# Kernel optimization log

Measured on AMD Instinct MI355X. Metric: run time of the kernel, lower is better.

The kernel has to match this reference:

```python
import jax, jax.numpy as jnp
import numpy as np

N, F, HOPS, HID, NCLS = 100000, 128, 8, 256, 64

def prelu(x, a):
    return jnp.where(x >= 0, x, a * x)

def setup_inputs() -> dict:
    key = jax.random.key(0)
    ks = jax.random.split(key, 8)
    w = lambda i, shape: (jax.random.normal(ks[i], shape, dtype=jnp.float32) * 0.02)
    return {
        "feats": jax.random.normal(ks[0], (HOPS, N, F), dtype=jnp.float32),
        # lr_jk_ref: Dense(HOPS*F, HID) -> PReLU(a_jk) -> Dense(HID, HID)
        "W_jk1": w(1, (HOPS * F, HID)), "b_jk1": jnp.zeros((HID,), jnp.float32),
        "W_jk2": w(2, (HID, HID)),      "b_jk2": jnp.zeros((HID,), jnp.float32),
        # PReLU params (nn.PReLU default init 0.25): FFN-internal, module-level, output-FFN
        "a_jk": jnp.float32(0.25), "a_main": jnp.float32(0.25), "a_out": jnp.float32(0.25),
        # lr_att: Linear(HID + F, 1), split into the jk_ref part and the per-hop x part
        "w_att_ref": w(3, (HID,)), "w_att_x": w(4, (F,)), "b_att": jnp.zeros((), jnp.float32),
        # lr_output: Dense(F, HID) -> PReLU(a_out) -> Dense(HID, NCLS)
        "W_o1": w(5, (F, HID)),  "b_o1": jnp.zeros((HID,), jnp.float32),
        "W_o2": w(6, (HID, NCLS)), "b_o2": jnp.zeros((NCLS,), jnp.float32),
    }

def reference(feats, W_jk1, b_jk1, W_jk2, b_jk2, a_jk, a_main, a_out,
              w_att_ref, w_att_x, b_att, W_o1, b_o1, W_o2, b_o2):
    # feats: [HOPS, N, F]; dropouts are identity (rates = 0 / eval mode)
    n = feats.shape[1]
    # torch.cat(input_list, dim=1) -> [N, HOPS*F]
    concat = jnp.transpose(feats, (1, 0, 2)).reshape(n, -1)
    # lr_jk_ref (FeedForwardNetII, n_layers=2): Dense -> PReLU -> Dense, then module PReLU
    h = prelu(concat @ W_jk1 + b_jk1, a_jk)
    jk_ref = prelu(h @ W_jk2 + b_jk2, a_main)              # [N, HID]
    # attention scores: sigmoid(Linear(cat(jk_ref, x_i))) for each hop i, vectorized
    s_ref = jk_ref @ w_att_ref                              # [N]
    s_x = jnp.einsum('hnf,f->nh', feats, w_att_x)           # [N, HOPS]
    scores = jax.nn.sigmoid(s_x + s_ref[:, None] + b_att)   # [N, HOPS]
    Wsm = jax.nn.softmax(scores, axis=1)                    # softmax over hops
    # weighted multi-hop aggregation: sum_i W[:,i] * x_i
    agg = jnp.einsum('nh,hnf->nf', Wsm, feats)              # [N, F]
    # lr_output (FeedForwardNetII, n_layers=2): Dense -> PReLU -> Dense
    out = prelu(agg @ W_o1 + b_o1, a_out) @ W_o2 + b_o2     # [N, NCLS]
    return out
```

## Files before the change

### kernel.cpp

```cpp
#include <hip/hip_runtime.h>
#include <hip/hip_bf16.h>
#include <cstdint>
#include <cstddef>

#define N_F 128
#define N_HOPS 8
#define N_HID 256
#define N_CLS 64

typedef __bf16 bf16;
typedef __attribute__((ext_vector_type(8))) __bf16 bf16x8;
typedef __attribute__((ext_vector_type(4))) float f32x4;

__device__ inline f32x4 mfma16(bf16x8 a, bf16x8 b, f32x4 c) {
    return __builtin_amdgcn_mfma_f32_16x16x32_bf16(a, b, c, 0, 0, 0);
}

typedef const __attribute__((address_space(1))) unsigned int guint;
typedef __attribute__((address_space(3))) unsigned int luint;
__device__ __forceinline__ void gl_lds16(const void* g, void* l) {
    __builtin_amdgcn_global_load_lds((guint*)g, (luint*)l, 16, 0, 0);
}

__device__ inline void pack_one(const float* __restrict__ s, bf16* __restrict__ d,
                                int NC, int ntn, int idx) {
    const int lane = idx & 63;
    const int f = idx >> 6;
    const int kt = f / ntn, nt = f - kt * ntn;
    const int krow = kt * 32 + ((lane >> 4) << 3);
    const int col = nt * 16 + (lane & 15);
    const float* ss = s + (size_t)krow * NC + col;
    bf16* dd = d + ((size_t)f * 64 + lane) * 8;
#pragma unroll
    for (int j = 0; j < 8; ++j) dd[j] = (bf16)ss[(size_t)j * NC];
}

__global__ void pack_weights(const float* __restrict__ W1, const float* __restrict__ W2,
                             const float* __restrict__ O1, const float* __restrict__ O2,
                             bf16* p1, bf16* p2, bf16* p3, bf16* p4) {
    int i = blockIdx.x * 256 + threadIdx.x;
    if (i < 32768) { pack_one(W1, p1, 256, 16, i); return; }
    i -= 32768;
    if (i < 8192)  { pack_one(W2, p2, 256, 16, i); return; }
    i -= 8192;
    if (i < 4096)  { pack_one(O1, p3, 256, 16, i); return; }
    i -= 4096;
    if (i < 2048)  { pack_one(O2, p4, 64, 4, i); return; }
}

__global__ __launch_bounds__(256) void k1_kernel(
    const float* __restrict__ feats, const bf16* __restrict__ w1p, const bf16* __restrict__ w2p,
    const float* __restrict__ b1, const float* __restrict__ b2,
    const float* __restrict__ a_jk_p, const float* __restrict__ a_main_p,
    const float* __restrict__ wref, const float* __restrict__ wax,
    const float* __restrict__ batt_p,
    float* __restrict__ wsm, int N)
{
    union __align__(16) U1 {
        struct { bf16 A[2048]; bf16 B[8192]; } s;
        bf16 H[64 * 264];
    };
    __shared__ U1 u;
    __shared__ float sx[64 * 8];
    __shared__ float sref[64];

    const int t = threadIdx.x;
    const int lane = t & 63;
    const int wc = t >> 6;
    const int row0 = blockIdx.x * 64;

    for (int i = t; i < 64 * 8; i += 256) sx[i] = 0.f;
    if (t < 64) sref[t] = 0.f;
    __syncthreads();

    const int srow = t & 63;
    const int sc = t >> 6;
    const int grow = min(row0 + srow, N - 1);

    f32x4 acc[4][4] = {};
    float pacc = 0.f;

    for (int kt = 0; kt < 32; ++kt) {
        const int h = kt >> 2;
        const int f0 = ((kt & 3) << 5) + (sc << 3);
        const float* srcp = feats + ((size_t)h * N + grow) * N_F + f0;
        const float4 v0 = *(const float4*)srcp;
        const float4 v1 = *(const float4*)(srcp + 4);
        pacc += v0.x * wax[f0]     + v0.y * wax[f0 + 1] + v0.z * wax[f0 + 2] + v0.w * wax[f0 + 3]
              + v1.x * wax[f0 + 4] + v1.y * wax[f0 + 5] + v1.z * wax[f0 + 6] + v1.w * wax[f0 + 7];
        if ((kt & 3) == 3) { atomicAdd(&sx[srow * 8 + h], pacc); pacc = 0.f; }
        bf16x8 av;
        av[0] = (bf16)v0.x; av[1] = (bf16)v0.y; av[2] = (bf16)v0.z; av[3] = (bf16)v0.w;
        av[4] = (bf16)v1.x; av[5] = (bf16)v1.y; av[6] = (bf16)v1.z; av[7] = (bf16)v1.w;
        *(bf16x8*)&u.s.A[((((srow >> 4) << 6) + (sc << 4) + (srow & 15))) << 3] = av;
        const bf16* bsrc = w1p + (size_t)kt * 8192;
#pragma unroll
        for (int r = 0; r < 4; ++r)
            gl_lds16(bsrc + r * 2048 + t * 8, &u.s.B[r * 2048 + t * 8]);
        __syncthreads();
        bf16x8 af[4], bfr[4];
#pragma unroll
        for (int i = 0; i < 4; ++i) af[i] = *(bf16x8*)&u.s.A[((i << 6) + lane) << 3];
#pragma unroll
        for (int j = 0; j < 4; ++j) bfr[j] = *(bf16x8*)&u.s.B[(((wc << 2) + j) * 64 + lane) << 3];
#pragma unroll
        for (int i = 0; i < 4; ++i)
#pragma unroll
            for (int j = 0; j < 4; ++j)
                acc[i][j] = mfma16(af[i], bfr[j], acc[i][j]);
        __syncthreads();
    }

    const float ajk = *a_jk_p;
#pragma unroll
    for (int j = 0; j < 4; ++j) {
        const int colg = (wc << 6) + (j << 4) + (lane & 15);
        const float bias = b1[colg];
#pragma unroll
        for (int i = 0; i < 4; ++i)
#pragma unroll
            for (int r = 0; r < 4; ++r) {
                const int row = (i << 4) + ((lane >> 4) << 2) + r;
                float v = acc[i][j][r] + bias;
                v = v >= 0.f ? v : ajk * v;
                u.H[row * 264 + colg] = (bf16)v;
            }
    }
    __syncthreads();

    f32x4 acc2[4][4] = {};
    for (int kt = 0; kt < 8; ++kt) {
        bf16x8 af[4], bfr[4];
#pragma unroll
        for (int i = 0; i < 4; ++i)
            af[i] = *(bf16x8*)&u.H[((i << 4) + (lane & 15)) * 264 + (kt << 5) + ((lane >> 4) << 3)];
#pragma unroll
        for (int j = 0; j < 4; ++j)
            bfr[j] = *(const bf16x8*)&w2p[((size_t)((kt << 4) + (wc << 2) + j) * 64 + lane) * 8];
#pragma unroll
        for (int i = 0; i < 4; ++i)
#pragma unroll
            for (int j = 0; j < 4; ++j)
                acc2[i][j] = mfma16(af[i], bfr[j], acc2[i][j]);
    }

    const float amain = *a_main_p;
    float pr[4][4] = {};
#pragma unroll
    for (int j = 0; j < 4; ++j) {
        const int colg = (wc << 6) + (j << 4) + (lane & 15);
        const float bias = b2[colg];
        const float wr_ = wref[colg];
#pragma unroll
        for (int i = 0; i < 4; ++i)
#pragma unroll
            for (int r = 0; r < 4; ++r) {
                float v = acc2[i][j][r] + bias;
                v = v >= 0.f ? v : amain * v;
                pr[i][r] += v * wr_;
            }
    }
#pragma unroll
    for (int m = 1; m < 16; m <<= 1)
#pragma unroll
        for (int i = 0; i < 4; ++i)
#pragma unroll
            for (int r = 0; r < 4; ++r)
                pr[i][r] += __shfl_xor(pr[i][r], m, 64);
    if ((lane & 15) == 0) {
#pragma unroll
        for (int i = 0; i < 4; ++i)
#pragma unroll
            for (int r = 0; r < 4; ++r)
                atomicAdd(&sref[(i << 4) + ((lane >> 4) << 2) + r], pr[i][r]);
    }
    __syncthreads();

    if (t < 64) {
        const int rg = row0 + t;
        if (rg < N) {
            const float sr = sref[t] + *batt_p;
            float e[8], mx = -1e30f;
#pragma unroll
            for (int h = 0; h < 8; ++h) {
                const float s = 1.f / (1.f + expf(-(sx[t * 8 + h] + sr)));
                e[h] = s; mx = fmaxf(mx, s);
            }
            float sum = 0.f;
#pragma unroll
            for (int h = 0; h < 8; ++h) { e[h] = expf(e[h] - mx); sum += e[h]; }
            const float inv = 1.f / sum;
#pragma unroll
            for (int h = 0; h < 8; ++h) wsm[(size_t)rg * 8 + h] = e[h] * inv;
        }
    }
}

__global__ __launch_bounds__(256) void k2_kernel(
    const float* __restrict__ feats, const float* __restrict__ wsm,
    const bf16* __restrict__ o1p, const bf16* __restrict__ o2p,
    const float* __restrict__ bo1, const float* __restrict__ a_out_p,
    const float* __restrict__ bo2, float* __restrict__ out, int N)
{
    union __align__(16) U2 {
        bf16 AG[64 * 136];
        bf16 HO[64 * 264];
    };
    __shared__ U2 u;
    __shared__ float wsl[512];

    const int t = threadIdx.x;
    const int lane = t & 63;
    const int cg = t >> 6;
    const int row0 = blockIdx.x * 64;

    for (int i = t; i < 512; i += 256) {
        const int rg = min(row0 + (i >> 3), N - 1);
        wsl[i] = wsm[(size_t)rg * 8 + (i & 7)];
    }
    __syncthreads();

    {
        const int r = t >> 2;
        const int c = t & 3;
        const int rg = min(row0 + r, N - 1);
        f32x4 a4[8] = {};
#pragma unroll
        for (int h = 0; h < 8; ++h) {
            const float wgt = wsl[r * 8 + h];
            const f32x4* p4 = (const f32x4*)(feats + ((size_t)h * N + rg) * N_F + c * 32);
#pragma unroll
            for (int q = 0; q < 8; ++q) a4[q] += wgt * p4[q];
        }
#pragma unroll
        for (int q2 = 0; q2 < 4; ++q2) {
            bf16x8 av;
#pragma unroll
            for (int e = 0; e < 4; ++e) {
                av[e] = (bf16)a4[q2 * 2][e];
                av[4 + e] = (bf16)a4[q2 * 2 + 1][e];
            }
            *(bf16x8*)&u.AG[r * 136 + c * 32 + q2 * 8] = av;
        }
    }
    __syncthreads();

    f32x4 acc3[4][4] = {};
    for (int kt = 0; kt < 4; ++kt) {
        bf16x8 af[4], bfr[4];
#pragma unroll
        for (int i = 0; i < 4; ++i)
            af[i] = *(bf16x8*)&u.AG[((i << 4) + (lane & 15)) * 136 + (kt << 5) + ((lane >> 4) << 3)];
#pragma unroll
        for (int j = 0; j < 4; ++j)
            bfr[j] = *(const bf16x8*)&o1p[((size_t)((kt << 4) + (cg << 2) + j) * 64 + lane) * 8];
#pragma unroll
        for (int i = 0; i < 4; ++i)
#pragma unroll
            for (int j = 0; j < 4; ++j)
                acc3[i][j] = mfma16(af[i], bfr[j], acc3[i][j]);
    }
    __syncthreads();

    const float aout = *a_out_p;
#pragma unroll
    for (int j = 0; j < 4; ++j) {
        const int colg = (cg << 6) + (j << 4) + (lane & 15);
        const float bias = bo1[colg];
#pragma unroll
        for (int i = 0; i < 4; ++i)
#pragma unroll
            for (int r = 0; r < 4; ++r) {
                const int row = (i << 4) + ((lane >> 4) << 2) + r;
                float v = acc3[i][j][r] + bias;
                v = v >= 0.f ? v : aout * v;
                u.HO[row * 264 + colg] = (bf16)v;
            }
    }
    __syncthreads();

    f32x4 acc4[4] = {};
    for (int kt = 0; kt < 8; ++kt) {
        const bf16x8 b = *(const bf16x8*)&o2p[((size_t)((kt << 2) + cg) * 64 + lane) * 8];
#pragma unroll
        for (int i = 0; i < 4; ++i) {
            const bf16x8 a = *(bf16x8*)&u.HO[((i << 4) + (lane & 15)) * 264 + (kt << 5) + ((lane >> 4) << 3)];
            acc4[i] = mfma16(a, b, acc4[i]);
        }
    }
    {
        const int colg = (cg << 4) + (lane & 15);
        const float bv = bo2[colg];
#pragma unroll
        for (int i = 0; i < 4; ++i)
#pragma unroll
            for (int r = 0; r < 4; ++r) {
                const int rg = row0 + (i << 4) + ((lane >> 4) << 2) + r;
                if (rg < N) out[(size_t)rg * 64 + colg] = acc4[i][r] + bv;
            }
    }
}

extern "C" void kernel_launch(void* const* d_in, const int* in_sizes, int n_in,
                              void* d_out, int out_size, void* d_ws, size_t ws_size,
                              hipStream_t stream) {
    const float* feats  = (const float*)d_in[0];
    const float* W1     = (const float*)d_in[1];
    const float* b1     = (const float*)d_in[2];
    const float* W2     = (const float*)d_in[3];
    const float* b2     = (const float*)d_in[4];
    const float* a_jk   = (const float*)d_in[5];
    const float* a_main = (const float*)d_in[6];
    const float* a_out  = (const float*)d_in[7];
    const float* wref   = (const float*)d_in[8];
    const float* wax    = (const float*)d_in[9];
    const float* batt   = (const float*)d_in[10];
    const float* O1     = (const float*)d_in[11];
    const float* bo1    = (const float*)d_in[12];
    const float* O2     = (const float*)d_in[13];
    const float* bo2    = (const float*)d_in[14];

    const int N = in_sizes[0] / (N_HOPS * N_F);

    char* ws = (char*)d_ws;
    bf16* p1 = (bf16*)ws;
    bf16* p2 = (bf16*)(ws + 524288);
    bf16* p3 = (bf16*)(ws + 655360);
    bf16* p4 = (bf16*)(ws + 720896);
    float* wsm = (float*)(ws + 753664);

    pack_weights<<<184, 256, 0, stream>>>(W1, W2, O1, O2, p1, p2, p3, p4);
    const int nb = (N + 63) / 64;
    k1_kernel<<<nb, 256, 0, stream>>>(feats, p1, p2, b1, b2, a_jk, a_main,
                                      wref, wax, batt, wsm, N);
    k2_kernel<<<nb, 256, 0, stream>>>(feats, wsm, p3, p4, bo1, a_out, bo2,
                                      (float*)d_out, N);
}
```

Baseline: 762.5 us.

## Load feats directly into MFMA fragments per wave and drop LDS staging in k1

In k1, each wave now loads its own A fragments of feats straight from global memory and its B fragments of W1 straight from global memory. This removes the shared A/B staging buffers and the two barriers per k-step. The attention dot product with w_att_x is split across waves by hop and reduced with shuffles instead of LDS atomics. The hidden activations in both kernels are stored in a fragment-ordered LDS layout so that MFMA operand reads become contiguous. The trade-off is that all four waves now read the same feats rows, giving 4x redundant global/L2 reads of the dominant input, in exchange for no block-level synchronization.

```diff
diff --git a/kernel.cpp b/kernel.cpp
--- a/kernel.cpp
+++ b/kernel.cpp
@@ -14,12 +14,6 @@
 
 __device__ inline f32x4 mfma16(bf16x8 a, bf16x8 b, f32x4 c) {
     return __builtin_amdgcn_mfma_f32_16x16x32_bf16(a, b, c, 0, 0, 0);
-}
-
-typedef const __attribute__((address_space(1))) unsigned int guint;
-typedef __attribute__((address_space(3))) unsigned int luint;
-__device__ __forceinline__ void gl_lds16(const void* g, void* l) {
-    __builtin_amdgcn_global_load_lds((guint*)g, (luint*)l, 16, 0, 0);
 }
 
 __device__ inline void pack_one(const float* __restrict__ s, bf16* __restrict__ d,
@@ -48,6 +42,10 @@
     if (i < 2048)  { pack_one(O2, p4, 64, 4, i); return; }
 }
 
+__device__ __forceinline__ int frag_addr(int row, int col) {
+    return (((col >> 5) << 2) + (row >> 4)) * 512 + (((row & 15) | (((col >> 3) & 3) << 4)) << 3) + (col & 7);
+}
+
 __global__ __launch_bounds__(256) void k1_kernel(
     const float* __restrict__ feats, const bf16* __restrict__ w1p, const bf16* __restrict__ w2p,
     const float* __restrict__ b1, const float* __restrict__ b2,
@@ -56,11 +54,7 @@
     const float* __restrict__ batt_p,
     float* __restrict__ wsm, int N)
 {
-    union __align__(16) U1 {
-        struct { bf16 A[2048]; bf16 B[8192]; } s;
-        bf16 H[64 * 264];
-    };
-    __shared__ U1 u;
+    __shared__ bf16 Hf[32 * 512];
     __shared__ float sx[64 * 8];
     __shared__ float sref[64];
 
@@ -68,62 +62,77 @@
     const int lane = t & 63;
     const int wc = t >> 6;
     const int row0 = blockIdx.x * 64;
-
-    for (int i = t; i < 64 * 8; i += 256) sx[i] = 0.f;
+    const int m = lane & 15, q = lane >> 4;
+
     if (t < 64) sref[t] = 0.f;
-    __syncthreads();
-
-    const int srow = t & 63;
-    const int sc = t >> 6;
-    const int grow = min(row0 + srow, N - 1);
+
+    size_t rbase[4];
+#pragma unroll
+    for (int i = 0; i < 4; ++i) {
+        const int r = min(row0 + (i << 4) + m, N - 1);
+        rbase[i] = (size_t)r * N_F;
+    }
 
     f32x4 acc[4][4] = {};
-    float pacc = 0.f;
+    float pacc[4] = {};
 
     for (int kt = 0; kt < 32; ++kt) {
         const int h = kt >> 2;
-        const int f0 = ((kt & 3) << 5) + (sc << 3);
-        const float* srcp = feats + ((size_t)h * N + grow) * N_F + f0;
-        const float4 v0 = *(const float4*)srcp;
-        const float4 v1 = *(const float4*)(srcp + 4);
-        pacc += v0.x * wax[f0]     + v0.y * wax[f0 + 1] + v0.z * wax[f0 + 2] + v0.w * wax[f0 + 3]
-              + v1.x * wax[f0 + 4] + v1.y * wax[f0 + 5] + v1.z * wax[f0 + 6] + v1.w * wax[f0 + 7];
-        if ((kt & 3) == 3) { atomicAdd(&sx[srow * 8 + h], pacc); pacc = 0.f; }
-        bf16x8 av;
-        av[0] = (bf16)v0.x; av[1] = (bf16)v0.y; av[2] = (bf16)v0.z; av[3] = (bf16)v0.w;
-        av[4] = (bf16)v1.x; av[5] = (bf16)v1.y; av[6] = (bf16)v1.z; av[7] = (bf16)v1.w;
-        *(bf16x8*)&u.s.A[((((srow >> 4) << 6) + (sc << 4) + (srow & 15))) << 3] = av;
-        const bf16* bsrc = w1p + (size_t)kt * 8192;
-#pragma unroll
-        for (int r = 0; r < 4; ++r)
-            gl_lds16(bsrc + r * 2048 + t * 8, &u.s.B[r * 2048 + t * 8]);
-        __syncthreads();
-        bf16x8 af[4], bfr[4];
-#pragma unroll
-        for (int i = 0; i < 4; ++i) af[i] = *(bf16x8*)&u.s.A[((i << 6) + lane) << 3];
-#pragma unroll
-        for (int j = 0; j < 4; ++j) bfr[j] = *(bf16x8*)&u.s.B[(((wc << 2) + j) * 64 + lane) << 3];
+        const int f0 = ((kt & 3) << 5) + (q << 3);
+        const size_t hoff = (size_t)h * N * N_F;
+        bf16x8 af[4];
+        float4 v0s[4], v1s[4];
+#pragma unroll
+        for (int i = 0; i < 4; ++i) {
+            const float* p = feats + hoff + rbase[i] + f0;
+            const float4 v0 = *(const float4*)p;
+            const float4 v1 = *(const float4*)(p + 4);
+            v0s[i] = v0; v1s[i] = v1;
+            af[i][0] = (bf16)v0.x; af[i][1] = (bf16)v0.y; af[i][2] = (bf16)v0.z; af[i][3] = (bf16)v0.w;
+            af[i][4] = (bf16)v1.x; af[i][5] = (bf16)v1.y; af[i][6] = (bf16)v1.z; af[i][7] = (bf16)v1.w;
+        }
+        bf16x8 bfr[4];
+#pragma unroll
+        for (int j = 0; j < 4; ++j)
+            bfr[j] = *(const bf16x8*)&w1p[((size_t)((kt << 4) + (wc << 2) + j) * 64 + lane) * 8];
 #pragma unroll
         for (int i = 0; i < 4; ++i)
 #pragma unroll
             for (int j = 0; j < 4; ++j)
                 acc[i][j] = mfma16(af[i], bfr[j], acc[i][j]);
-        __syncthreads();
+        if ((kt >> 3) == wc) {
+#pragma unroll
+            for (int i = 0; i < 4; ++i) {
+                const float4 v0 = v0s[i], v1 = v1s[i];
+                pacc[i] += v0.x * wax[f0]     + v0.y * wax[f0 + 1] + v0.z * wax[f0 + 2] + v0.w * wax[f0 + 3]
+                         + v1.x * wax[f0 + 4] + v1.y * wax[f0 + 5] + v1.z * wax[f0 + 6] + v1.w * wax[f0 + 7];
+            }
+            if ((kt & 3) == 3) {
+#pragma unroll
+                for (int i = 0; i < 4; ++i) {
+                    float v = pacc[i];
+                    v += __shfl_xor(v, 16);
+                    v += __shfl_xor(v, 32);
+                    if (lane < 16) sx[(((i << 4) + lane) << 3) + h] = v;
+                    pacc[i] = 0.f;
+                }
+            }
+        }
     }
 
     const float ajk = *a_jk_p;
 #pragma unroll
     for (int j = 0; j < 4; ++j) {
-        const int colg = (wc << 6) + (j << 4) + (lane & 15);
+        const int colg = (wc << 6) + (j << 4) + m;
         const float bias = b1[colg];
 #pragma unroll
         for (int i = 0; i < 4; ++i)
 #pragma unroll
             for (int r = 0; r < 4; ++r) {
-                const int row = (i << 4) + ((lane >> 4) << 2) + r;
+                const int row = (i << 4) + (q << 2) + r;
                 float v = acc[i][j][r] + bias;
                 v = v >= 0.f ? v : ajk * v;
-                u.H[row * 264 + colg] = (bf16)v;
+                Hf[frag_addr(row, colg)] = (bf16)v;
             }
     }
     __syncthreads();
@@ -133,7 +142,7 @@
         bf16x8 af[4], bfr[4];
 #pragma unroll
         for (int i = 0; i < 4; ++i)
-            af[i] = *(bf16x8*)&u.H[((i << 4) + (lane & 15)) * 264 + (kt << 5) + ((lane >> 4) << 3)];
+            af[i] = *(bf16x8*)&Hf[(((kt << 2) + i) << 9) + (lane << 3)];
 #pragma unroll
         for (int j = 0; j < 4; ++j)
             bfr[j] = *(const bf16x8*)&w2p[((size_t)((kt << 4) + (wc << 2) + j) * 64 + lane) * 8];
@@ -148,7 +157,7 @@
     float pr[4][4] = {};
 #pragma unroll
     for (int j = 0; j < 4; ++j) {
-        const int colg = (wc << 6) + (j << 4) + (lane & 15);
+        const int colg = (wc << 6) + (j << 4) + m;
         const float bias = b2[colg];
         const float wr_ = wref[colg];
 #pragma unroll
@@ -161,18 +170,18 @@
             }
     }
 #pragma unroll
-    for (int m = 1; m < 16; m <<= 1)
+    for (int mk = 1; mk < 16; mk <<= 1)
 #pragma unroll
         for (int i = 0; i < 4; ++i)
 #pragma unroll
             for (int r = 0; r < 4; ++r)
-                pr[i][r] += __shfl_xor(pr[i][r], m, 64);
-    if ((lane & 15) == 0) {
+                pr[i][r] += __shfl_xor(pr[i][r], mk, 64);
+    if (m == 0) {
 #pragma unroll
         for (int i = 0; i < 4; ++i)
 #pragma unroll
             for (int r = 0; r < 4; ++r)
-                atomicAdd(&sref[(i << 4) + ((lane >> 4) << 2) + r], pr[i][r]);
+                atomicAdd(&sref[(i << 4) + (q << 2) + r], pr[i][r]);
     }
     __syncthreads();
 
@@ -203,8 +212,8 @@
     const float* __restrict__ bo2, float* __restrict__ out, int N)
 {
     union __align__(16) U2 {
-        bf16 AG[64 * 136];
-        bf16 HO[64 * 264];
+        bf16 AGf[16 * 512];
+        bf16 HOf[32 * 512];
     };
     __shared__ U2 u;
     __shared__ float wsl[512];
@@ -213,6 +222,7 @@
     const int lane = t & 63;
     const int cg = t >> 6;
     const int row0 = blockIdx.x * 64;
+    const int m = lane & 15, q = lane >> 4;
 
     for (int i = t; i < 512; i += 256) {
         const int rg = min(row0 + (i >> 3), N - 1);
@@ -230,17 +240,14 @@
             const float wgt = wsl[r * 8 + h];
             const f32x4* p4 = (const f32x4*)(feats + ((size_t)h * N + rg) * N_F + c * 32);
 #pragma unroll
-            for (int q = 0; q < 8; ++q) a4[q] += wgt * p4[q];
-        }
-#pragma unroll
-        for (int q2 = 0; q2 < 4; ++q2) {
+            for (int qq = 0; qq < 8; ++qq) a4[qq] += wgt * p4[qq];
+        }
+#pragma unroll
+        for (int qq = 0; qq < 4; ++qq) {
             bf16x8 av;
 #pragma unroll
-            for (int e = 0; e < 4; ++e) {
-                av[e] = (bf16)a4[q2 * 2][e];
-                av[4 + e] = (bf16)a4[q2 * 2 + 1][e];
-            }
-            *(bf16x8*)&u.AG[r * 136 + c * 32 + q2 * 8] = av;
+            for (int e = 0; e < 8; ++e) av[e] = (bf16)a4[(qq << 1) + (e >> 2)][e & 3];
+            *(bf16x8*)&u.AGf[((((c << 2) + (r >> 4)) << 9) + (((r & 15) | (qq << 4)) << 3))] = av;
         }
     }
     __syncthreads();
@@ -250,7 +257,7 @@
         bf16x8 af[4], bfr[4];
 #pragma unroll
         for (int i = 0; i < 4; ++i)
-            af[i] = *(bf16x8*)&u.AG[((i << 4) + (lane & 15)) * 136 + (kt << 5) + ((lane >> 4) << 3)];
+            af[i] = *(bf16x8*)&u.AGf[(((kt << 2) + i) << 9) + (lane << 3)];
 #pragma unroll
         for (int j = 0; j < 4; ++j)
             bfr[j] = *(const bf16x8*)&o1p[((size_t)((kt << 4) + (cg << 2) + j) * 64 + lane) * 8];
@@ -265,16 +272,16 @@
     const float aout = *a_out_p;
 #pragma unroll
     for (int j = 0; j < 4; ++j) {
-        const int colg = (cg << 6) + (j << 4) + (lane & 15);
+        const int colg = (cg << 6) + (j << 4) + m;
         const float bias = bo1[colg];
 #pragma unroll
         for (int i = 0; i < 4; ++i)
 #pragma unroll
             for (int r = 0; r < 4; ++r) {
-                const int row = (i << 4) + ((lane >> 4) << 2) + r;
+                const int row = (i << 4) + (q << 2) + r;
                 float v = acc3[i][j][r] + bias;
                 v = v >= 0.f ? v : aout * v;
-                u.HO[row * 264 + colg] = (bf16)v;
+                u.HOf[frag_addr(row, colg)] = (bf16)v;
             }
     }
     __syncthreads();
@@ -284,18 +291,18 @@
         const bf16x8 b = *(const bf16x8*)&o2p[((size_t)((kt << 2) + cg) * 64 + lane) * 8];
 #pragma unroll
         for (int i = 0; i < 4; ++i) {
-            const bf16x8 a = *(bf16x8*)&u.HO[((i << 4) + (lane & 15)) * 264 + (kt << 5) + ((lane >> 4) << 3)];
+            const bf16x8 a = *(bf16x8*)&u.HOf[(((kt << 2) + i) << 9) + (lane << 3)];
             acc4[i] = mfma16(a, b, acc4[i]);
         }
     }
     {
-        const int colg = (cg << 4) + (lane & 15);
+        const int colg = (cg << 4) + m;
         const float bv = bo2[colg];
 #pragma unroll
         for (int i = 0; i < 4; ++i)
 #pragma unroll
             for (int r = 0; r < 4; ++r) {
-                const int rg = row0 + (i << 4) + ((lane >> 4) << 2) + r;
+                const int rg = row0 + (i << 4) + (q << 2) + r;
                 if (rg < N) out[(size_t)rg * 64 + colg] = acc4[i][r] + bv;
             }
     }
```

After: 810.6 us. +6.3%, slower.
